# Performance work log

Measured on AMD Instinct MI355X. Metric: run time of the kernel, lower is better.

The kernel has to match this reference:

```python
import jax, jax.numpy as jnp
import numpy as np

N_TASKS, N_DATA, N_DEV = 200000, 100000, 4
E_TD, E_TT, E_DV = 800000, 1600000, 800000
D_TASK, D_DATA, D_DEVF = 12, 5, 12
DE_TD, DE_TT, DE_DV = 3, 1, 2
C = 64  # hidden_channels, n_heads=1, concat=False


def setup_inputs() -> dict:
    key = jax.random.key(0)
    ks = iter(jax.random.split(key, 64))
    nrm = lambda shape, s=1.0: jax.random.normal(next(ks), shape, dtype=jnp.float32) * s
    ridx = lambda n, hi: jax.random.randint(next(ks), (n,), 0, hi, dtype=jnp.int32)
    inp = {
        "x_tasks": nrm((N_TASKS, D_TASK)),
        "x_data": nrm((N_DATA, D_DATA)),
        "x_devices": nrm((N_DEV, D_DEVF)),
        "src_td": ridx(E_TD, N_DATA), "dst_td": ridx(E_TD, N_TASKS), "eattr_td": nrm((E_TD, DE_TD)),
        "src_tt": ridx(E_TT, N_TASKS), "dst_tt": ridx(E_TT, N_TASKS), "eattr_tt": nrm((E_TT, DE_TT)),
        "src_dv": ridx(E_DV, N_DEV), "dst_dv": ridx(E_DV, N_TASKS), "eattr_dv": nrm((E_DV, DE_DV)),
    }
    # GATConv parameters per relation (H=1): lin_src, lin_dst, lin_edge, att vectors, residual lin, bias
    for tag, ds, de in (("td", D_DATA, DE_TD), ("tt", D_TASK, DE_TT), ("dv", D_DEVF, DE_DV)):
        inp[f"Ws_{tag}"] = nrm((ds, C), 0.1)
        inp[f"Wd_{tag}"] = nrm((D_TASK, C), 0.1)
        inp[f"We_{tag}"] = nrm((de, C), 0.1)
        inp[f"as_{tag}"] = nrm((C,), 0.1)
        inp[f"ad_{tag}"] = nrm((C,), 0.1)
        inp[f"ae_{tag}"] = nrm((C,), 0.1)
        inp[f"Wr_{tag}"] = nrm((D_TASK, C), 0.1)
        inp[f"b_{tag}"] = jnp.zeros((C,), jnp.float32)
    inp["ln_g"] = jnp.ones((D_TASK + 3 * C,), jnp.float32)
    inp["ln_b"] = jnp.zeros((D_TASK + 3 * C,), jnp.float32)
    return inp


def _gat(x_src, x_dst, src, dst, eattr, Ws, Wd, We, a_s, a_d, a_e, Wr, b, n_dst):
    # PyG GATConv: heads=1, concat=False, residual=True, add_self_loops=False, edge_dim set
    hs = x_src @ Ws                       # [Ns, C]
    hd = x_dst @ Wd                       # [Nd, C]
    he = eattr @ We                       # [E, C]
    logits = (hs @ a_s)[src] + (hd @ a_d)[dst] + he @ a_e   # [E]
    logits = jax.nn.leaky_relu(logits, 0.2)
    m = jax.ops.segment_max(logits, dst, num_segments=n_dst)
    m = jnp.where(jnp.isfinite(m), m, 0.0)                  # empty segments -> 0
    ex = jnp.exp(logits - m[dst])
    denom = jax.ops.segment_sum(ex, dst, num_segments=n_dst)
    coef = ex / (denom[dst] + 1e-16)                        # segment softmax over incoming edges
    out = jax.ops.segment_sum(coef[:, None] * hs[src], dst, num_segments=n_dst)  # [Nd, C]
    return out + x_dst @ Wr + b                             # residual + bias


def reference(x_tasks, x_data, x_devices,
              src_td, dst_td, eattr_td, src_tt, dst_tt, eattr_tt, src_dv, dst_dv, eattr_dv,
              Ws_td, Wd_td, We_td, as_td, ad_td, ae_td, Wr_td, b_td,
              Ws_tt, Wd_tt, We_tt, as_tt, ad_tt, ae_tt, Wr_tt, b_tt,
              Ws_dv, Wd_dv, We_dv, as_dv, ad_dv, ae_dv, Wr_dv, b_dv,
              ln_g, ln_b):
    o_td = _gat(x_data, x_tasks, src_td, dst_td, eattr_td, Ws_td, Wd_td, We_td, as_td, ad_td, ae_td, Wr_td, b_td, N_TASKS)
    o_tt = _gat(x_tasks, x_tasks, src_tt, dst_tt, eattr_tt, Ws_tt, Wd_tt, We_tt, as_tt, ad_tt, ae_tt, Wr_tt, b_tt, N_TASKS)
    o_dv = _gat(x_devices, x_tasks, src_dv, dst_dv, eattr_dv, Ws_dv, Wd_dv, We_dv, as_dv, ad_dv, ae_dv, Wr_dv, b_dv, N_TASKS)
    # HeteroConv aggr='cat' over the 3 relations, then skip-concat of raw task features
    x = jnp.concatenate([x_tasks, o_td, o_tt, o_dv], axis=-1)  # [N_tasks, 12+3*64]
    mu = jnp.mean(x, axis=-1, keepdims=True)
    var = jnp.var(x, axis=-1, keepdims=True)
    x = (x - mu) * jax.lax.rsqrt(var + 1e-5) * ln_g + ln_b
    return jax.nn.leaky_relu(x, 0.01)
```

## Files before the change

kernel.cpp:

```cpp
#include <hip/hip_runtime.h>
#include <math.h>

#define N_TASKS 200000
#define N_DATA  100000
#define N_DEV   4
#define E_TD    800000
#define E_TT    1600000
#define E_DV    800000
#define E_ALL   (E_TD + E_TT + E_DV)

struct __align__(8) Payload { int src; float scal; };

#define OFF_HS_TD   0
#define OFF_HS_TT   (OFF_HS_TD + 6400000)
#define OFF_HS_DV   (OFF_HS_TT + 12800000)
#define OFF_SS_TD   (OFF_HS_DV + 256)
#define OFF_SS_TT   (OFF_SS_TD + 100000)
#define OFF_SS_DV   (OFF_SS_TT + 200000)
#define OFF_WDAD    (OFF_SS_DV + 8)
#define OFF_WEA     (OFF_WDAD + 64)
#define OFF_CNT     (OFF_WEA + 8)
#define OFF_PTR     (OFF_CNT + 600000)
#define OFF_AUX     (OFF_PTR + 600000)
#define OFF_PAY     (OFF_AUX + 1024)
#define SCAN_N      600000
#define SCAN_BLOCKS ((SCAN_N + 1023) / 1024)

#define CNT_B   12500
#define HS_TD_B 25000
#define HS_TT_B 50000
#define PRE_B   (CNT_B + HS_TD_B + HS_TT_B + 1)

__global__ void prep_kernel(const float* Wd_td, const float* ad_td,
                            const float* Wd_tt, const float* ad_tt,
                            const float* Wd_dv, const float* ad_dv,
                            const float* We_td, const float* ae_td,
                            const float* We_tt, const float* ae_tt,
                            const float* We_dv, const float* ae_dv,
                            float* wdad, float* wea) {
    int t = threadIdx.x;
    if (t < 36) {
        int r = t / 12, k = t % 12;
        const float* Wd = r == 0 ? Wd_td : (r == 1 ? Wd_tt : Wd_dv);
        const float* ad = r == 0 ? ad_td : (r == 1 ? ad_tt : ad_dv);
        float acc = 0.f;
        for (int c = 0; c < 64; ++c) acc += Wd[k * 64 + c] * ad[c];
        wdad[r * 12 + k] = acc;
    } else if (t < 42) {
        int i = t - 36;
        int r, k;
        if (i < 3)      { r = 0; k = i; }
        else if (i < 4) { r = 1; k = 0; }
        else            { r = 2; k = i - 4; }
        const float* We = r == 0 ? We_td : (r == 1 ? We_tt : We_dv);
        const float* ae = r == 0 ? ae_td : (r == 1 ? ae_tt : ae_dv);
        float acc = 0.f;
        for (int c = 0; c < 64; ++c) acc += We[k * 64 + c] * ae[c];
        wea[i] = acc;
    }
}

template <int DS>
__device__ __forceinline__ void hs_body(const float* __restrict__ x, int Ns,
                                        const float* __restrict__ Ws, const float* __restrict__ a_s,
                                        float* __restrict__ hs, float* __restrict__ ss,
                                        int blk, int tid) {
    int gid = blk * 256 + tid;
    int s = gid >> 6;
    int lane = gid & 63;
    if (s >= Ns) return;
    float xv[DS];
    #pragma unroll
    for (int k = 0; k < DS; ++k) xv[k] = x[(size_t)s * DS + k];
    float acc = 0.f;
    #pragma unroll
    for (int k = 0; k < DS; ++k) acc = fmaf(xv[k], Ws[k * 64 + lane], acc);
    hs[(size_t)s * 64 + lane] = acc;
    float t = acc * a_s[lane];
    for (int off = 32; off; off >>= 1) t += __shfl_down(t, off, 64);
    if (lane == 0) ss[s] = t;
}

__global__ __launch_bounds__(256) void pre_kernel(
    const float* __restrict__ x_data, const float* __restrict__ x_tasks, const float* __restrict__ x_devices,
    const float* __restrict__ Ws_td, const float* __restrict__ as_td,
    const float* __restrict__ Ws_tt, const float* __restrict__ as_tt,
    const float* __restrict__ Ws_dv, const float* __restrict__ as_dv,
    float* __restrict__ hs_td, float* __restrict__ ss_td,
    float* __restrict__ hs_tt, float* __restrict__ ss_tt,
    float* __restrict__ hs_dv, float* __restrict__ ss_dv,
    const int* __restrict__ dst_td, const int* __restrict__ dst_tt, const int* __restrict__ dst_dv,
    int* __restrict__ cnt) {
    int b = blockIdx.x, tid = threadIdx.x;
    if (b < CNT_B) {
        int i = b * 256 + tid;
        if (i < E_TD) {
            atomicAdd(&cnt[dst_td[i]], 1);
        } else if (i < E_TD + E_TT) {
            atomicAdd(&cnt[N_TASKS + dst_tt[i - E_TD]], 1);
        } else if (i < E_ALL) {
            atomicAdd(&cnt[2 * N_TASKS + dst_dv[i - E_TD - E_TT]], 1);
        }
        return;
    }
    b -= CNT_B;
    if (b < HS_TD_B) { hs_body<5>(x_data, N_DATA, Ws_td, as_td, hs_td, ss_td, b, tid); return; }
    b -= HS_TD_B;
    if (b < HS_TT_B) { hs_body<12>(x_tasks, N_TASKS, Ws_tt, as_tt, hs_tt, ss_tt, b, tid); return; }
    b -= HS_TT_B;
    hs_body<12>(x_devices, N_DEV, Ws_dv, as_dv, hs_dv, ss_dv, 0, tid);
}

__global__ void scan1(const int* __restrict__ cnt, int* __restrict__ ptr,
                      int* __restrict__ aux, int n) {
    __shared__ int s[256];
    int b = blockIdx.x, t = threadIdx.x;
    int base = b * 1024 + t * 4;
    int v0 = base + 0 < n ? cnt[base + 0] : 0;
    int v1 = base + 1 < n ? cnt[base + 1] : 0;
    int v2 = base + 2 < n ? cnt[base + 2] : 0;
    int v3 = base + 3 < n ? cnt[base + 3] : 0;
    int tsum = v0 + v1 + v2 + v3;
    s[t] = tsum;
    __syncthreads();
    for (int off = 1; off < 256; off <<= 1) {
        int x = (t >= off) ? s[t - off] : 0;
        __syncthreads();
        s[t] += x;
        __syncthreads();
    }
    int p = s[t] - tsum;
    if (t == 255) aux[b] = s[255];
    if (base + 0 < n) ptr[base + 0] = p; p += v0;
    if (base + 1 < n) ptr[base + 1] = p; p += v1;
    if (base + 2 < n) ptr[base + 2] = p; p += v2;
    if (base + 3 < n) ptr[base + 3] = p;
}

__global__ void scan2(int* __restrict__ aux, int nb) {
    __shared__ int s[256];
    int t = threadIdx.x;
    int carry = 0;
    for (int base = 0; base < nb; base += 256) {
        int i = base + t;
        int v = i < nb ? aux[i] : 0;
        s[t] = v;
        __syncthreads();
        for (int off = 1; off < 256; off <<= 1) {
            int x = (t >= off) ? s[t - off] : 0;
            __syncthreads();
            s[t] += x;
            __syncthreads();
        }
        int excl = s[t] - v + carry;
        if (i < nb) aux[i] = excl;
        int total = s[255];
        __syncthreads();
        carry += total;
    }
}

__global__ void scatter_all(const int* __restrict__ src_td, const int* __restrict__ dst_td, const float* __restrict__ ea_td,
                            const int* __restrict__ src_tt, const int* __restrict__ dst_tt, const float* __restrict__ ea_tt,
                            const int* __restrict__ src_dv, const int* __restrict__ dst_dv, const float* __restrict__ ea_dv,
                            const float* __restrict__ wea,
                            const float* __restrict__ ss_td, const float* __restrict__ ss_tt, const float* __restrict__ ss_dv,
                            int* __restrict__ cursor, const int* __restrict__ aux,
                            Payload* __restrict__ payload) {
    int i = blockIdx.x * blockDim.x + threadIdx.x;
    if (i >= E_ALL) return;
    int s, dseg;
    float sc;
    if (i < E_TD) {
        int e = i;
        sc = ea_td[(size_t)e * 3 + 0] * wea[0] + ea_td[(size_t)e * 3 + 1] * wea[1] + ea_td[(size_t)e * 3 + 2] * wea[2];
        s = src_td[e];
        sc += ss_td[s];
        dseg = dst_td[e];
    } else if (i < E_TD + E_TT) {
        int e = i - E_TD;
        sc = ea_tt[e] * wea[3];
        s = src_tt[e];
        sc += ss_tt[s];
        dseg = N_TASKS + dst_tt[e];
    } else {
        int e = i - E_TD - E_TT;
        sc = ea_dv[(size_t)e * 2 + 0] * wea[4] + ea_dv[(size_t)e * 2 + 1] * wea[5];
        s = src_dv[e];
        sc += ss_dv[s];
        dseg = 2 * N_TASKS + dst_dv[e];
    }
    int pos = atomicAdd(&cursor[dseg], 1) + aux[dseg >> 10];
    Payload p; p.src = s; p.scal = sc;
    payload[pos] = p;
}

__device__ __forceinline__ float gat_wave(
    int d, int r, int lane,
    const int* __restrict__ ptr, const int* __restrict__ cnt, const int* __restrict__ aux,
    const Payload* __restrict__ payload,
    const float* __restrict__ hs, const float* __restrict__ Wr, const float* __restrict__ bb,
    const float* __restrict__ xp, const float* __restrict__ wdad) {
    int idx = r * N_TASKS + d;
    int end = ptr[idx] + aux[idx >> 10];
    int beg = end - cnt[idx];
    float c = 0.f;
    #pragma unroll
    for (int k = 0; k < 12; ++k) c = fmaf(xp[k], wdad[r * 12 + k], c);
    float acc = 0.f, wsum = 0.f;
    #pragma unroll 4
    for (int e = beg; e < end; ++e) {
        Payload p = payload[e];
        float sc = p.scal + c;
        float lg = sc > 0.f ? sc : 0.2f * sc;
        float w = __expf(lg);
        acc = fmaf(w, hs[(size_t)p.src * 64 + lane], acc);
        wsum += w;
    }
    float res = bb[lane];
    #pragma unroll
    for (int k = 0; k < 12; ++k) res = fmaf(xp[k], Wr[k * 64 + lane], res);
    return acc / (wsum + 1e-16f) + res;
}

__global__ __launch_bounds__(256) void fused_node_kernel(
    const float* __restrict__ x_tasks,
    const int* __restrict__ ptr, const int* __restrict__ cnt, const int* __restrict__ aux,
    const Payload* __restrict__ payload,
    const float* __restrict__ hs_td, const float* __restrict__ hs_tt, const float* __restrict__ hs_dv,
    const float* __restrict__ wdad,
    const float* __restrict__ Wr_td, const float* __restrict__ Wr_tt, const float* __restrict__ Wr_dv,
    const float* __restrict__ b_td, const float* __restrict__ b_tt, const float* __restrict__ b_dv,
    const float* __restrict__ ln_g, const float* __restrict__ ln_b,
    float* __restrict__ out) {
    int wid = (blockIdx.x * blockDim.x + threadIdx.x) >> 6;
    if (wid >= N_TASKS) return;
    int d = __builtin_amdgcn_readfirstlane(wid);
    int lane = threadIdx.x & 63;

    const float* xp = x_tasks + (size_t)d * 12;
    float xl = lane < 12 ? xp[lane] : 0.f;

    float a0 = gat_wave(d, 0, lane, ptr, cnt, aux, payload, hs_td, Wr_td, b_td, xp, wdad);
    float a1 = gat_wave(d, 1, lane, ptr, cnt, aux, payload, hs_tt, Wr_tt, b_tt, xp, wdad);
    float a2 = gat_wave(d, 2, lane, ptr, cnt, aux, payload, hs_dv, Wr_dv, b_dv, xp, wdad);

    float sum = a0 + a1 + a2 + xl;
    float sq  = a0 * a0 + a1 * a1 + a2 * a2 + xl * xl;
    #pragma unroll
    for (int off = 1; off < 64; off <<= 1) {
        sum += __shfl_xor(sum, off, 64);
        sq  += __shfl_xor(sq, off, 64);
    }
    float mu = sum * (1.f / 204.f);
    float rstd = rsqrtf(sq * (1.f / 204.f) - mu * mu + 1e-5f);

    float* op = out + (size_t)d * 204;
    if (lane < 12) {
        float y = (xl - mu) * rstd * ln_g[lane] + ln_b[lane];
        op[lane] = y > 0.f ? y : 0.01f * y;
    }
    {
        float y = (a0 - mu) * rstd * ln_g[12 + lane] + ln_b[12 + lane];
        op[12 + lane] = y > 0.f ? y : 0.01f * y;
    }
    {
        float y = (a1 - mu) * rstd * ln_g[76 + lane] + ln_b[76 + lane];
        op[76 + lane] = y > 0.f ? y : 0.01f * y;
    }
    {
        float y = (a2 - mu) * rstd * ln_g[140 + lane] + ln_b[140 + lane];
        op[140 + lane] = y > 0.f ? y : 0.01f * y;
    }
}

extern "C" void kernel_launch(void* const* d_in, const int* in_sizes, int n_in,
                              void* d_out, int out_size, void* d_ws, size_t ws_size,
                              hipStream_t stream) {
    const float* x_tasks   = (const float*)d_in[0];
    const float* x_data    = (const float*)d_in[1];
    const float* x_devices = (const float*)d_in[2];
    const int*   src_td = (const int*)d_in[3];
    const int*   dst_td = (const int*)d_in[4];
    const float* eattr_td = (const float*)d_in[5];
    const int*   src_tt = (const int*)d_in[6];
    const int*   dst_tt = (const int*)d_in[7];
    const float* eattr_tt = (const float*)d_in[8];
    const int*   src_dv = (const int*)d_in[9];
    const int*   dst_dv = (const int*)d_in[10];
    const float* eattr_dv = (const float*)d_in[11];
    const float* Ws_td = (const float*)d_in[12];
    const float* Wd_td = (const float*)d_in[13];
    const float* We_td = (const float*)d_in[14];
    const float* as_td = (const float*)d_in[15];
    const float* ad_td = (const float*)d_in[16];
    const float* ae_td = (const float*)d_in[17];
    const float* Wr_td = (const float*)d_in[18];
    const float* b_td  = (const float*)d_in[19];
    const float* Ws_tt = (const float*)d_in[20];
    const float* Wd_tt = (const float*)d_in[21];
    const float* We_tt = (const float*)d_in[22];
    const float* as_tt = (const float*)d_in[23];
    const float* ad_tt = (const float*)d_in[24];
    const float* ae_tt = (const float*)d_in[25];
    const float* Wr_tt = (const float*)d_in[26];
    const float* b_tt  = (const float*)d_in[27];
    const float* Ws_dv = (const float*)d_in[28];
    const float* Wd_dv = (const float*)d_in[29];
    const float* We_dv = (const float*)d_in[30];
    const float* as_dv = (const float*)d_in[31];
    const float* ad_dv = (const float*)d_in[32];
    const float* ae_dv = (const float*)d_in[33];
    const float* Wr_dv = (const float*)d_in[34];
    const float* b_dv  = (const float*)d_in[35];
    const float* ln_g  = (const float*)d_in[36];
    const float* ln_b  = (const float*)d_in[37];

    float* ws = (float*)d_ws;
    float* hs_td = ws + OFF_HS_TD;
    float* hs_tt = ws + OFF_HS_TT;
    float* hs_dv = ws + OFF_HS_DV;
    float* ss_td = ws + OFF_SS_TD;
    float* ss_tt = ws + OFF_SS_TT;
    float* ss_dv = ws + OFF_SS_DV;
    float* wdad  = ws + OFF_WDAD;
    float* wea   = ws + OFF_WEA;
    int*   cnt   = (int*)(ws + OFF_CNT);
    int*   ptr   = (int*)(ws + OFF_PTR);
    int*   aux   = (int*)(ws + OFF_AUX);
    Payload* pay = (Payload*)(ws + OFF_PAY);

    float* outp = (float*)d_out;

    hipMemsetAsync(cnt, 0, SCAN_N * sizeof(int), stream);

    prep_kernel<<<1, 64, 0, stream>>>(Wd_td, ad_td, Wd_tt, ad_tt, Wd_dv, ad_dv,
                                      We_td, ae_td, We_tt, ae_tt, We_dv, ae_dv,
                                      wdad, wea);

    pre_kernel<<<PRE_B, 256, 0, stream>>>(
        x_data, x_tasks, x_devices,
        Ws_td, as_td, Ws_tt, as_tt, Ws_dv, as_dv,
        hs_td, ss_td, hs_tt, ss_tt, hs_dv, ss_dv,
        dst_td, dst_tt, dst_dv, cnt);

    scan1<<<SCAN_BLOCKS, 256, 0, stream>>>(cnt, ptr, aux, SCAN_N);
    scan2<<<1, 256, 0, stream>>>(aux, SCAN_BLOCKS);

    scatter_all<<<(E_ALL + 255) / 256, 256, 0, stream>>>(
        src_td, dst_td, eattr_td, src_tt, dst_tt, eattr_tt, src_dv, dst_dv, eattr_dv,
        wea, ss_td, ss_tt, ss_dv, ptr, aux, pay);

    fused_node_kernel<<<(N_TASKS * 64 + 255) / 256, 256, 0, stream>>>(
        x_tasks, ptr, cnt, aux, pay, hs_td, hs_tt, hs_dv, wdad,
        Wr_td, Wr_tt, Wr_dv, b_td, b_tt, b_dv, ln_g, ln_b, outp);
}
```

Baseline: 794.1 us.

## Record edge ranks at count time, precompute exp weights in scatter, fold memset

The counting pass now stores each edge's atomic rank, so the scatter pass computes its slot from ptr+aux+rank instead of issuing a second atomic on a cursor. The per-destination dot product (x·Wd·ad) is precomputed per node in extra scan1 blocks, and scatter stores the final exp(leaky_relu(logit)) weight, so the per-wave edge loop only does the FMAs. The memset is folded into the prep kernel. Rank and sdv scratch live in the output buffer, which is overwritten afterwards. This avoids the unnormalised softmax's max subtraction, as the old code already did, so it carries the same overflow risk.

```diff
diff --git a/kernel.cpp b/kernel.cpp
--- a/kernel.cpp
+++ b/kernel.cpp
@@ -31,14 +31,26 @@
 #define HS_TT_B 50000
 #define PRE_B   (CNT_B + HS_TD_B + HS_TT_B + 1)
 
-__global__ void prep_kernel(const float* Wd_td, const float* ad_td,
+#define SDV_B   782
+
+#define PREP_B  (1 + SCAN_BLOCKS)
+
+__global__ __launch_bounds__(256) void prep_kernel(
+                            const float* Wd_td, const float* ad_td,
                             const float* Wd_tt, const float* ad_tt,
                             const float* Wd_dv, const float* ad_dv,
                             const float* We_td, const float* ae_td,
                             const float* We_tt, const float* ae_tt,
                             const float* We_dv, const float* ae_dv,
-                            float* wdad, float* wea) {
-    int t = threadIdx.x;
+                            float* wdad, float* wea, int* cnt) {
+    int b = blockIdx.x, t = threadIdx.x;
+    if (b > 0) {
+        int base = (b - 1) * 1024 + t * 4;
+        #pragma unroll
+        for (int k = 0; k < 4; ++k)
+            if (base + k < SCAN_N) cnt[base + k] = 0;
+        return;
+    }
     if (t < 36) {
         int r = t / 12, k = t % 12;
         const float* Wd = r == 0 ? Wd_td : (r == 1 ? Wd_tt : Wd_dv);
@@ -90,17 +102,16 @@
     float* __restrict__ hs_tt, float* __restrict__ ss_tt,
     float* __restrict__ hs_dv, float* __restrict__ ss_dv,
     const int* __restrict__ dst_td, const int* __restrict__ dst_tt, const int* __restrict__ dst_dv,
-    int* __restrict__ cnt) {
+    int* __restrict__ cnt, int* __restrict__ rank_buf) {
     int b = blockIdx.x, tid = threadIdx.x;
     if (b < CNT_B) {
         int i = b * 256 + tid;
-        if (i < E_TD) {
-            atomicAdd(&cnt[dst_td[i]], 1);
-        } else if (i < E_TD + E_TT) {
-            atomicAdd(&cnt[N_TASKS + dst_tt[i - E_TD]], 1);
-        } else if (i < E_ALL) {
-            atomicAdd(&cnt[2 * N_TASKS + dst_dv[i - E_TD - E_TT]], 1);
-        }
+        int dseg;
+        if (i < E_TD)               dseg = dst_td[i];
+        else if (i < E_TD + E_TT)   dseg = N_TASKS + dst_tt[i - E_TD];
+        else if (i < E_ALL)         dseg = 2 * N_TASKS + dst_dv[i - E_TD - E_TT];
+        else return;
+        rank_buf[i] = atomicAdd(&cnt[dseg], 1);
         return;
     }
     b -= CNT_B;
@@ -111,10 +122,29 @@
     hs_body<12>(x_devices, N_DEV, Ws_dv, as_dv, hs_dv, ss_dv, 0, tid);
 }
 
-__global__ void scan1(const int* __restrict__ cnt, int* __restrict__ ptr,
-                      int* __restrict__ aux, int n) {
+__global__ __launch_bounds__(256) void scan1(
+    const int* __restrict__ cnt, int* __restrict__ ptr,
+    int* __restrict__ aux, int n,
+    const float* __restrict__ x_tasks, const float* __restrict__ wdad,
+    float* __restrict__ sdv) {
     __shared__ int s[256];
     int b = blockIdx.x, t = threadIdx.x;
+    if (b >= SCAN_BLOCKS) {
+        int d = (b - SCAN_BLOCKS) * 256 + t;
+        if (d < N_TASKS) {
+            float xv[12];
+            #pragma unroll
+            for (int k = 0; k < 12; ++k) xv[k] = x_tasks[(size_t)d * 12 + k];
+            #pragma unroll
+            for (int r = 0; r < 3; ++r) {
+                float acc = 0.f;
+                #pragma unroll
+                for (int k = 0; k < 12; ++k) acc = fmaf(xv[k], wdad[r * 12 + k], acc);
+                sdv[r * N_TASKS + d] = acc;
+            }
+        }
+        return;
+    }
     int base = b * 1024 + t * 4;
     int v0 = base + 0 < n ? cnt[base + 0] : 0;
     int v1 = base + 1 < n ? cnt[base + 1] : 0;
@@ -165,7 +195,8 @@
                             const int* __restrict__ src_dv, const int* __restrict__ dst_dv, const float* __restrict__ ea_dv,
                             const float* __restrict__ wea,
                             const float* __restrict__ ss_td, const float* __restrict__ ss_tt, const float* __restrict__ ss_dv,
-                            int* __restrict__ cursor, const int* __restrict__ aux,
+                            const int* __restrict__ ptr, const int* __restrict__ aux,
+                            const int* __restrict__ rank_buf, const float* __restrict__ sdv,
                             Payload* __restrict__ payload) {
     int i = blockIdx.x * blockDim.x + threadIdx.x;
     if (i >= E_ALL) return;
@@ -190,8 +221,10 @@
         sc += ss_dv[s];
         dseg = 2 * N_TASKS + dst_dv[e];
     }
-    int pos = atomicAdd(&cursor[dseg], 1) + aux[dseg >> 10];
-    Payload p; p.src = s; p.scal = sc;
+    sc += sdv[dseg];
+    float lg = sc > 0.f ? sc : 0.2f * sc;
+    int pos = ptr[dseg] + aux[dseg >> 10] + rank_buf[i];
+    Payload p; p.src = s; p.scal = __expf(lg);
     payload[pos] = p;
 }
 
@@ -200,22 +233,16 @@
     const int* __restrict__ ptr, const int* __restrict__ cnt, const int* __restrict__ aux,
     const Payload* __restrict__ payload,
     const float* __restrict__ hs, const float* __restrict__ Wr, const float* __restrict__ bb,
-    const float* __restrict__ xp, const float* __restrict__ wdad) {
+    const float* __restrict__ xp) {
     int idx = r * N_TASKS + d;
-    int end = ptr[idx] + aux[idx >> 10];
-    int beg = end - cnt[idx];
-    float c = 0.f;
-    #pragma unroll
-    for (int k = 0; k < 12; ++k) c = fmaf(xp[k], wdad[r * 12 + k], c);
+    int beg = ptr[idx] + aux[idx >> 10];
+    int end = beg + cnt[idx];
     float acc = 0.f, wsum = 0.f;
     #pragma unroll 4
     for (int e = beg; e < end; ++e) {
         Payload p = payload[e];
-        float sc = p.scal + c;
-        float lg = sc > 0.f ? sc : 0.2f * sc;
-        float w = __expf(lg);
-        acc = fmaf(w, hs[(size_t)p.src * 64 + lane], acc);
-        wsum += w;
+        acc = fmaf(p.scal, hs[(size_t)p.src * 64 + lane], acc);
+        wsum += p.scal;
     }
     float res = bb[lane];
     #pragma unroll
@@ -228,7 +255,6 @@
     const int* __restrict__ ptr, const int* __restrict__ cnt, const int* __restrict__ aux,
     const Payload* __restrict__ payload,
     const float* __restrict__ hs_td, const float* __restrict__ hs_tt, const float* __restrict__ hs_dv,
-    const float* __restrict__ wdad,
     const float* __restrict__ Wr_td, const float* __restrict__ Wr_tt, const float* __restrict__ Wr_dv,
     const float* __restrict__ b_td, const float* __restrict__ b_tt, const float* __restrict__ b_dv,
     const float* __restrict__ ln_g, const float* __restrict__ ln_b,
@@ -241,9 +267,9 @@
     const float* xp = x_tasks + (size_t)d * 12;
     float xl = lane < 12 ? xp[lane] : 0.f;
 
-    float a0 = gat_wave(d, 0, lane, ptr, cnt, aux, payload, hs_td, Wr_td, b_td, xp, wdad);
-    float a1 = gat_wave(d, 1, lane, ptr, cnt, aux, payload, hs_tt, Wr_tt, b_tt, xp, wdad);
-    float a2 = gat_wave(d, 2, lane, ptr, cnt, aux, payload, hs_dv, Wr_dv, b_dv, xp, wdad);
+    float a0 = gat_wave(d, 0, lane, ptr, cnt, aux, payload, hs_td, Wr_td, b_td, xp);
+    float a1 = gat_wave(d, 1, lane, ptr, cnt, aux, payload, hs_tt, Wr_tt, b_tt, xp);
+    float a2 = gat_wave(d, 2, lane, ptr, cnt, aux, payload, hs_dv, Wr_dv, b_dv, xp);
 
     float sum = a0 + a1 + a2 + xl;
     float sq  = a0 * a0 + a1 * a1 + a2 * a2 + xl * xl;
@@ -331,27 +357,27 @@
     Payload* pay = (Payload*)(ws + OFF_PAY);
 
     float* outp = (float*)d_out;
-
-    hipMemsetAsync(cnt, 0, SCAN_N * sizeof(int), stream);
-
-    prep_kernel<<<1, 64, 0, stream>>>(Wd_td, ad_td, Wd_tt, ad_tt, Wd_dv, ad_dv,
-                                      We_td, ae_td, We_tt, ae_tt, We_dv, ae_dv,
-                                      wdad, wea);
+    int*   rank_buf = (int*)d_out;
+    float* sdv      = (float*)d_out + E_ALL;
+
+    prep_kernel<<<PREP_B, 256, 0, stream>>>(Wd_td, ad_td, Wd_tt, ad_tt, Wd_dv, ad_dv,
+                                            We_td, ae_td, We_tt, ae_tt, We_dv, ae_dv,
+                                            wdad, wea, cnt);
 
     pre_kernel<<<PRE_B, 256, 0, stream>>>(
         x_data, x_tasks, x_devices,
         Ws_td, as_td, Ws_tt, as_tt, Ws_dv, as_dv,
         hs_td, ss_td, hs_tt, ss_tt, hs_dv, ss_dv,
-        dst_td, dst_tt, dst_dv, cnt);
-
-    scan1<<<SCAN_BLOCKS, 256, 0, stream>>>(cnt, ptr, aux, SCAN_N);
+        dst_td, dst_tt, dst_dv, cnt, rank_buf);
+
+    scan1<<<SCAN_BLOCKS + SDV_B, 256, 0, stream>>>(cnt, ptr, aux, SCAN_N, x_tasks, wdad, sdv);
     scan2<<<1, 256, 0, stream>>>(aux, SCAN_BLOCKS);
 
     scatter_all<<<(E_ALL + 255) / 256, 256, 0, stream>>>(
         src_td, dst_td, eattr_td, src_tt, dst_tt, eattr_tt, src_dv, dst_dv, eattr_dv,
-        wea, ss_td, ss_tt, ss_dv, ptr, aux, pay);
+        wea, ss_td, ss_tt, ss_dv, ptr, aux, rank_buf, sdv, pay);
 
     fused_node_kernel<<<(N_TASKS * 64 + 255) / 256, 256, 0, stream>>>(
-        x_tasks, ptr, cnt, aux, pay, hs_td, hs_tt, hs_dv, wdad,
+        x_tasks, ptr, cnt, aux, pay, hs_td, hs_tt, hs_dv,
         Wr_td, Wr_tt, Wr_dv, b_td, b_tt, b_dv, ln_g, ln_b, outp);
 }
```

After: 745.1 us. 6.2% less time.
